# Performance work log

Hardware: AMD Instinct MI355X
Metric: run time of the kernel (lower is better)

## Reference

```python
import jax, jax.numpy as jnp
import numpy as np
from jax import lax

B, S, H, T = 64, 512, 1024, 48


def setup_inputs() -> dict:
    key = jax.random.key(0)
    ks = jax.random.split(key, 8)
    x = jax.random.normal(ks[0], (B, S, H), dtype=jnp.float32)
    # left-aligned variable-length attention mask (lengths in [S//2, S])
    lengths = jax.random.randint(ks[1], (B,), S // 2, S + 1)
    attention_mask = (jnp.arange(S)[None, :] < lengths[:, None]).astype(jnp.int32)
    labels = jax.random.randint(ks[2], (B, S), 0, T).astype(jnp.int64)
    # decoder Linear(H, T)
    W = jax.random.normal(ks[3], (H, T), dtype=jnp.float32) / np.sqrt(H)
    b = jnp.zeros((T,), dtype=jnp.float32)
    # CRF parameters (allennlp-style: transitions + start/end transitions)
    transitions = jax.random.normal(ks[4], (T, T), dtype=jnp.float32) * 0.1
    start_trans = jax.random.normal(ks[5], (T,), dtype=jnp.float32) * 0.1
    end_trans = jax.random.normal(ks[6], (T,), dtype=jnp.float32) * 0.1
    return {"x": x, "attention_mask": attention_mask, "labels": labels,
            "W": W, "b": b, "transitions": transitions,
            "start_trans": start_trans, "end_trans": end_trans}


def _log_partition(logits, mask, trans, start, end):
    # logits [B,S,T], mask [B,S] int. Returns logZ [B].
    alpha0 = start[None, :] + logits[:, 0]                     # [B,T]
    emits = jnp.moveaxis(logits[:, 1:], 1, 0)                  # [S-1,B,T]
    ms = mask[:, 1:].T                                         # [S-1,B]

    def step(alpha, inp):
        emit, m = inp
        inner = alpha[:, :, None] + trans[None, :, :] + emit[:, None, :]  # [B,T,T]
        new = jax.nn.logsumexp(inner, axis=1)
        alpha = jnp.where(m[:, None] > 0, new, alpha)
        return alpha, None

    alpha, _ = lax.scan(step, alpha0, (emits, ms))
    return jax.nn.logsumexp(alpha + end[None, :], axis=1)      # [B]


def _gold_score(logits, labels, mask, trans, start, end):
    maskf = mask.astype(logits.dtype)
    emit = jnp.take_along_axis(logits, labels[..., None], axis=2)[..., 0]  # [B,S]
    emit_score = jnp.sum(emit * maskf, axis=1)
    tr = trans[labels[:, :-1], labels[:, 1:]]                   # [B,S-1]
    trans_score = jnp.sum(tr * maskf[:, 1:], axis=1)
    last_idx = jnp.sum(mask, axis=1) - 1                        # [B]
    last_tags = jnp.take_along_axis(labels, last_idx[:, None], axis=1)[:, 0]
    return start[labels[:, 0]] + emit_score + trans_score + end[last_tags]


def _viterbi(logits, mask, trans, start, end):
    Bn, Sn, Tn = logits.shape
    v0 = start[None, :] + logits[:, 0]
    emits = jnp.moveaxis(logits[:, 1:], 1, 0)                  # [S-1,B,T]
    ms = mask[:, 1:].T
    ident = jnp.broadcast_to(jnp.arange(Tn, dtype=jnp.int32)[None, :], (Bn, Tn))

    def step(v, inp):
        emit, m = inp
        scores = v[:, :, None] + trans[None, :, :]              # [B,T_prev,T_cur]
        bp = jnp.argmax(scores, axis=1).astype(jnp.int32)       # [B,T]
        best = jnp.max(scores, axis=1) + emit
        v_new = jnp.where(m[:, None] > 0, best, v)
        bp = jnp.where(m[:, None] > 0, bp, ident)               # identity at padded steps
        return v_new, bp

    v, bps = lax.scan(step, v0, (emits, ms))                    # bps [S-1,B,T]
    last = jnp.argmax(v + end[None, :], axis=1).astype(jnp.int32)  # [B]

    def back(tag, bp):
        prev = jnp.take_along_axis(bp, tag[:, None], axis=1)[:, 0]
        return prev, tag

    first_tag, rest = lax.scan(back, last, bps, reverse=True)   # rest [S-1,B]
    tags = jnp.concatenate([first_tag[:, None], rest.T], axis=1)  # [B,S]
    return (tags * mask).astype(jnp.int64)                      # pad with zeros


def reference(x, attention_mask, labels, W, b, transitions, start_trans, end_trans):
    features = jnp.einsum('bsh,ht->bst', x, W) + b              # decoder Linear
    pred_labels = _viterbi(features, attention_mask, transitions, start_trans, end_trans)
    logZ = _log_partition(features, attention_mask, transitions, start_trans, end_trans)
    gold = _gold_score(features, labels, attention_mask, transitions, start_trans, end_trans)
    loss = -jnp.sum(gold - logZ)                                # -log-likelihood, summed over batch
    return features, pred_labels, loss
```

## Files before the change

kernel.cpp:

```cpp
#include <hip/hip_runtime.h>
#include <hip/hip_bf16.h>
#include <math.h>

#define Bn 64
#define Sn 512
#define Hn 1024
#define Tn 48

#define LOG2E 1.4426950408889634f
#define LN2f  0.6931471805599453f

#define PRED_OFF (Bn*Sn*Tn)
#define LOSS_OFF (PRED_OFF + Bn*Sn)

#define RL(x,i) __int_as_float(__builtin_amdgcn_readlane(__float_as_int(x),(i)))

#if __has_builtin(__builtin_amdgcn_exp2f)
#define EXP2(x) __builtin_amdgcn_exp2f(x)
#else
#define EXP2(x) exp2f(x)
#endif
#if __has_builtin(__builtin_amdgcn_logf)
#define LOG2(x) __builtin_amdgcn_logf(x)
#else
#define LOG2(x) log2f(x)
#endif

__device__ __forceinline__ unsigned umin2(unsigned a, unsigned b) { return a < b ? a : b; }

#define VWS_BYTE_OFF 512
#define BPW_BYTE_OFF (512 + (size_t)Bn*Sn*Tn*4)

#define DOT4(ACC,A,B) { ACC = fmaf((A).x,(B).x,ACC); ACC = fmaf((A).y,(B).y,ACC); ACC = fmaf((A).z,(B).z,ACC); ACC = fmaf((A).w,(B).w,ACC); }

__global__ __launch_bounds__(256) void gemm_feat(
    const float* __restrict__ x, const float* __restrict__ W,
    const float* __restrict__ bias, float* __restrict__ feat)
{
  __shared__ __align__(16) float xs[128][68];
  __shared__ __align__(16) float wsT[Tn][68];
  const int tid = threadIdx.x;
  const int srow  = tid >> 1;
  const int shalf = tid & 1;
  const int ty = tid >> 3;
  const int tx = tid & 7;
  const size_t row0 = (size_t)blockIdx.x * 128;

  float4 xreg[8];
  float  wreg[12];
  #pragma unroll
  for (int p = 0; p < 8; ++p)
    xreg[p] = *reinterpret_cast<const float4*>(&x[(row0 + srow)*Hn + shalf*32 + p*4]);
  #pragma unroll
  for (int i = 0; i < 12; ++i) {
    const int id = tid + i*256; const int kk = id/Tn; const int t = id - kk*Tn;
    wreg[i] = W[(size_t)kk*Tn + t];
  }

  float acc[4][6];
  #pragma unroll
  for (int r = 0; r < 4; ++r)
    #pragma unroll
    for (int c = 0; c < 6; ++c) acc[r][c] = 0.f;

  for (int k0 = 0; k0 < Hn; k0 += 64) {
    #pragma unroll
    for (int p = 0; p < 8; ++p)
      *reinterpret_cast<float4*>(&xs[srow][shalf*32 + p*4]) = xreg[p];
    #pragma unroll
    for (int i = 0; i < 12; ++i) {
      const int id = tid + i*256; const int kk = id/Tn; const int t = id - kk*Tn;
      wsT[t][kk] = wreg[i];
    }
    __syncthreads();
    if (k0 + 64 < Hn) {
      #pragma unroll
      for (int p = 0; p < 8; ++p)
        xreg[p] = *reinterpret_cast<const float4*>(&x[(row0 + srow)*Hn + (k0+64) + shalf*32 + p*4]);
      #pragma unroll
      for (int i = 0; i < 12; ++i) {
        const int id = tid + i*256; const int kk = id/Tn; const int t = id - kk*Tn;
        wreg[i] = W[(size_t)(k0 + 64 + kk)*Tn + t];
      }
    }
    #pragma unroll 4
    for (int kk = 0; kk < 64; kk += 4) {
      const float4 a0 = *reinterpret_cast<const float4*>(&xs[ty +  0][kk]);
      const float4 a1 = *reinterpret_cast<const float4*>(&xs[ty + 32][kk]);
      const float4 a2 = *reinterpret_cast<const float4*>(&xs[ty + 64][kk]);
      const float4 a3 = *reinterpret_cast<const float4*>(&xs[ty + 96][kk]);
      const float4 w0 = *reinterpret_cast<const float4*>(&wsT[tx*6+0][kk]);
      const float4 w1 = *reinterpret_cast<const float4*>(&wsT[tx*6+1][kk]);
      const float4 w2 = *reinterpret_cast<const float4*>(&wsT[tx*6+2][kk]);
      const float4 w3 = *reinterpret_cast<const float4*>(&wsT[tx*6+3][kk]);
      const float4 w4 = *reinterpret_cast<const float4*>(&wsT[tx*6+4][kk]);
      const float4 w5 = *reinterpret_cast<const float4*>(&wsT[tx*6+5][kk]);
      DOT4(acc[0][0],a0,w0) DOT4(acc[0][1],a0,w1) DOT4(acc[0][2],a0,w2)
      DOT4(acc[0][3],a0,w3) DOT4(acc[0][4],a0,w4) DOT4(acc[0][5],a0,w5)
      DOT4(acc[1][0],a1,w0) DOT4(acc[1][1],a1,w1) DOT4(acc[1][2],a1,w2)
      DOT4(acc[1][3],a1,w3) DOT4(acc[1][4],a1,w4) DOT4(acc[1][5],a1,w5)
      DOT4(acc[2][0],a2,w0) DOT4(acc[2][1],a2,w1) DOT4(acc[2][2],a2,w2)
      DOT4(acc[2][3],a2,w3) DOT4(acc[2][4],a2,w4) DOT4(acc[2][5],a2,w5)
      DOT4(acc[3][0],a3,w0) DOT4(acc[3][1],a3,w1) DOT4(acc[3][2],a3,w2)
      DOT4(acc[3][3],a3,w3) DOT4(acc[3][4],a3,w4) DOT4(acc[3][5],a3,w5)
    }
    __syncthreads();
  }
  #pragma unroll
  for (int c = 0; c < 6; ++c) {
    const int col = tx*6 + c;
    const float bv = bias[col];
    #pragma unroll
    for (int r = 0; r < 4; ++r)
      feat[(row0 + ty + r*32)*Tn + col] = acc[r][c] + bv;
  }
}

__device__ __forceinline__ int seq_len(const int* __restrict__ mask, int b, int lane) {
  int lc = 0;
  #pragma unroll
  for (int it = 0; it < Sn/64; ++it) lc += (mask[(size_t)b*Sn + it*64 + lane] != 0);
  #pragma unroll
  for (int off = 32; off; off >>= 1) lc += __shfl_xor(lc, off);
  return lc;
}

__global__ __launch_bounds__(64, 1) void crf_scan(
    const float* __restrict__ feat,
    const int* __restrict__ mask,
    const int* __restrict__ labels,
    const float* __restrict__ trans,
    const float* __restrict__ startv,
    const float* __restrict__ endv,
    float* __restrict__ vws,
    float* __restrict__ wsLogZ,
    float* __restrict__ wsGold)
{
  const int role = blockIdx.x >> 6;
  const int b    = blockIdx.x & 63;
  const int lane = threadIdx.x;
  const float* fb = feat + (size_t)b * Sn * Tn;
  const int len = seq_len(mask, b, lane);
  const int j = (lane < Tn) ? lane : (Tn - 1);

  if (role == 0) {
    float4 E0,E1,E2,E3,E4,E5,E6,E7,E8,E9,E10,E11;
    #define LDE(k) E##k.x = EXP2(trans[(4*k+0)*Tn + j]*LOG2E); \
                   E##k.y = EXP2(trans[(4*k+1)*Tn + j]*LOG2E); \
                   E##k.z = EXP2(trans[(4*k+2)*Tn + j]*LOG2E); \
                   E##k.w = EXP2(trans[(4*k+3)*Tn + j]*LOG2E);
    LDE(0) LDE(1) LDE(2) LDE(3) LDE(4) LDE(5) LDE(6) LDE(7) LDE(8) LDE(9) LDE(10) LDE(11)
    #undef LDE
    float emq0,emq1,emq2,emq3,emq4,emq5,emq6,emq7;
    #define LDEM(u) { int s = 1 + u; s = s < len ? s : len - 1; emq##u = fb[(size_t)s*Tn + j]; }
    LDEM(0) LDEM(1) LDEM(2) LDEM(3) LDEM(4) LDEM(5) LDEM(6) LDEM(7)
    #undef LDEM
    const float a0 = (startv[j] + fb[j]) * LOG2E;
    float Zref = RL(a0, 0);
    float beta = a0 - Zref;
    float p = EXP2(beta);
    #define FMAG(k) \
      s0 = fmaf(RL(p,4*k+0), E##k.x, s0); \
      s1 = fmaf(RL(p,4*k+1), E##k.y, s1); \
      s2 = fmaf(RL(p,4*k+2), E##k.z, s2); \
      s3 = fmaf(RL(p,4*k+3), E##k.w, s3);
    #define PSTEP(u) { const int tt = t + u; if (tt < len) { \
      const float em2 = emq##u * LOG2E; \
      int tf = tt + 8; tf = tf < len ? tf : len - 1; \
      emq##u = fb[(size_t)tf * Tn + j]; \
      float s0=0.f,s1=0.f,s2=0.f,s3=0.f; \
      FMAG(0) FMAG(1) FMAG(2) FMAG(3) FMAG(4) FMAG(5) \
      FMAG(6) FMAG(7) FMAG(8) FMAG(9) FMAG(10) FMAG(11) \
      const float dj = LOG2((s0+s1)+(s2+s3)) + em2; \
      const float d0 = RL(dj,0); \
      Zref += d0; beta = dj - d0; p = EXP2(beta); } }
    for (int t = 1; t < len; t += 8) {
      PSTEP(0) PSTEP(1) PSTEP(2) PSTEP(3) PSTEP(4) PSTEP(5) PSTEP(6) PSTEP(7)
    }
    #undef PSTEP
    #undef FMAG
    float fv = (lane < Tn) ? beta + endv[lane] * LOG2E : -INFINITY;
    float m = fv;
    #pragma unroll
    for (int off = 32; off; off >>= 1) m = fmaxf(m, __shfl_xor(m, off));
    float e = (lane < Tn) ? EXP2(fv - m) : 0.f;
    #pragma unroll
    for (int off = 32; off; off >>= 1) e += __shfl_xor(e, off);
    if (lane == 0) wsLogZ[b] = (Zref + m + LOG2(e)) * LN2f;

  } else if (role == 1) {
    float4 T0,T1,T2,T3,T4,T5,T6,T7,T8,T9,T10,T11;
    #define LDT(k) T##k.x = trans[(4*k+0)*Tn + j]; \
                   T##k.y = trans[(4*k+1)*Tn + j]; \
                   T##k.z = trans[(4*k+2)*Tn + j]; \
                   T##k.w = trans[(4*k+3)*Tn + j];
    LDT(0) LDT(1) LDT(2) LDT(3) LDT(4) LDT(5) LDT(6) LDT(7) LDT(8) LDT(9) LDT(10) LDT(11)
    #undef LDT
    float emq0,emq1,emq2,emq3,emq4,emq5,emq6,emq7;
    #define LDEM(u) { int s = 1 + u; s = s < len ? s : len - 1; emq##u = fb[(size_t)s*Tn + j]; }
    LDEM(0) LDEM(1) LDEM(2) LDEM(3) LDEM(4) LDEM(5) LDEM(6) LDEM(7)
    #undef LDEM
    float v = startv[j] + fb[j];
    if (lane < Tn) vws[(size_t)b*Sn*Tn + lane] = v;
    #define MAXG(k) const float g##k = fmaxf( \
      fmaxf(RL(v,4*k+0)+T##k.x, RL(v,4*k+1)+T##k.y), \
      fmaxf(RL(v,4*k+2)+T##k.z, RL(v,4*k+3)+T##k.w));
    #define VSTEP(u) { const int tt = t + u; if (tt < len) { \
      const float em_cur = emq##u; \
      int tf = tt + 8; tf = tf < len ? tf : len - 1; \
      emq##u = fb[(size_t)tf * Tn + j]; \
      MAXG(0) MAXG(1) MAXG(2) MAXG(3) MAXG(4) MAXG(5) \
      MAXG(6) MAXG(7) MAXG(8) MAXG(9) MAXG(10) MAXG(11) \
      const float h0 = fmaxf(fmaxf(g0,g1),fmaxf(g2,g3)); \
      const float h1 = fmaxf(fmaxf(g4,g5),fmaxf(g6,g7)); \
      const float h2 = fmaxf(fmaxf(g8,g9),fmaxf(g10,g11)); \
      const float best = fmaxf(fmaxf(h0,h1),h2); \
      v = best + em_cur; \
      if (lane < Tn) vws[((size_t)b*Sn + tt)*Tn + lane] = v; } }
    for (int t = 1; t < len; t += 8) {
      VSTEP(0) VSTEP(1) VSTEP(2) VSTEP(3) VSTEP(4) VSTEP(5) VSTEP(6) VSTEP(7)
    }
    #undef VSTEP
    #undef MAXG

  } else {
    float g = 0.f;
    #pragma unroll
    for (int it = 0; it < Sn/64; ++it) {
      const int sg = it*64 + lane;
      if (sg < len) {
        const int la = labels[(size_t)b*Sn + sg];
        float e = fb[(size_t)sg*Tn + la];
        if (sg > 0) e += trans[labels[(size_t)b*Sn + sg - 1]*Tn + la];
        g += e;
      }
    }
    #pragma unroll
    for (int off = 32; off; off >>= 1) g += __shfl_xor(g, off);
    if (lane == 0) {
      g += startv[labels[(size_t)b*Sn]] + endv[labels[(size_t)b*Sn + len - 1]];
      wsGold[b] = g;
    }
  }
}

__global__ __launch_bounds__(256) void bp_kernel(
    const float* __restrict__ vws,
    const int* __restrict__ mask,
    const float* __restrict__ trans,
    unsigned char* __restrict__ bpw)
{
  const int b    = blockIdx.x >> 3;
  const int oct  = blockIdx.x & 7;
  const int wv   = threadIdx.x >> 6;
  const int lane = threadIdx.x & 63;
  const int len = seq_len(mask, b, lane);
  const int j = (lane < Tn) ? lane : (Tn - 1);

  float4 T0,T1,T2,T3,T4,T5,T6,T7,T8,T9,T10,T11;
  #define LDT(k) T##k.x = trans[(4*k+0)*Tn + j]; \
                 T##k.y = trans[(4*k+1)*Tn + j]; \
                 T##k.z = trans[(4*k+2)*Tn + j]; \
                 T##k.w = trans[(4*k+3)*Tn + j];
  LDT(0) LDT(1) LDT(2) LDT(3) LDT(4) LDT(5) LDT(6) LDT(7) LDT(8) LDT(9) LDT(10) LDT(11)
  #undef LDT

  const int t0 = oct*64 + wv*16;
  for (int i = 0; i < 16; ++i) {
    const int t = t0 + i;
    int te = t; te = te < 1 ? 1 : te; te = te < len ? te : len - 1;
    const float4* vp = reinterpret_cast<const float4*>(vws + ((size_t)b*Sn + te - 1)*Tn);
    #define LDA(k) const float4 A##k = vp[k];
    LDA(0) LDA(1) LDA(2) LDA(3) LDA(4) LDA(5) LDA(6) LDA(7) LDA(8) LDA(9) LDA(10) LDA(11)
    #undef LDA
    #define GMAX(k) const float gq##k = fmaxf( \
      fmaxf(A##k.x+T##k.x, A##k.y+T##k.y), fmaxf(A##k.z+T##k.z, A##k.w+T##k.w));
    GMAX(0) GMAX(1) GMAX(2) GMAX(3) GMAX(4) GMAX(5)
    GMAX(6) GMAX(7) GMAX(8) GMAX(9) GMAX(10) GMAX(11)
    #undef GMAX
    const float h0 = fmaxf(fmaxf(gq0,gq1),fmaxf(gq2,gq3));
    const float h1 = fmaxf(fmaxf(gq4,gq5),fmaxf(gq6,gq7));
    const float h2 = fmaxf(fmaxf(gq8,gq9),fmaxf(gq10,gq11));
    const float best = fmaxf(fmaxf(h0,h1),h2);
    #define KEYG(k) umin2( \
      umin2(__float_as_uint((A##k.x+T##k.x)-best)|(unsigned)(4*k+0), \
            __float_as_uint((A##k.y+T##k.y)-best)|(unsigned)(4*k+1)), \
      umin2(__float_as_uint((A##k.z+T##k.z)-best)|(unsigned)(4*k+2), \
            __float_as_uint((A##k.w+T##k.w)-best)|(unsigned)(4*k+3)))
    const unsigned kA = umin2(umin2(KEYG(0), KEYG(1)), umin2(KEYG(2), KEYG(3)));
    const unsigned kB = umin2(umin2(KEYG(4), KEYG(5)), umin2(KEYG(6), KEYG(7)));
    const unsigned kC = umin2(umin2(KEYG(8), KEYG(9)), umin2(KEYG(10), KEYG(11)));
    #undef KEYG
    const unsigned bidx = umin2(umin2(kA, kB), kC);
    if (t >= 1 && t < len && lane < Tn)
      bpw[((size_t)b*Sn + t)*Tn + lane] = (unsigned char)bidx;
  }
}

__device__ __forceinline__ unsigned idw(int a) {
  return (unsigned)a | ((unsigned)(a+1)<<8) | ((unsigned)(a+2)<<16) | ((unsigned)(a+3)<<24);
}

__global__ __launch_bounds__(64, 1) void backtrace_kernel(
    const float* __restrict__ vws,
    const unsigned char* __restrict__ bpw,
    const int* __restrict__ mask,
    const float* __restrict__ endv,
    float* __restrict__ pred_out)
{
  __shared__ unsigned char bpL[Sn * Tn];
  __shared__ unsigned char pathL[384 * 64];
  __shared__ int EA[8];

  const int b    = blockIdx.x;
  const int lane = threadIdx.x;
  const int len = seq_len(mask, b, lane);

  {
    const uint4* gb = reinterpret_cast<const uint4*>(bpw + (size_t)b*Sn*Tn);
    uint4* bl = reinterpret_cast<uint4*>(bpL);
    for (int i4 = lane; i4 < Sn*Tn/16; i4 += 64) {
      const int byte0 = i4*16;
      const int t = byte0 / Tn;
      const int j0 = byte0 - t*Tn;
      uint4 val;
      if (t >= 1 && t < len) val = gb[i4];
      else { val.x = idw(j0); val.y = idw(j0+4); val.z = idw(j0+8); val.w = idw(j0+12); }
      bl[i4] = val;
    }
  }

  float fv = (lane < Tn) ? vws[((size_t)b*Sn + len - 1)*Tn + lane] + endv[lane] : -INFINITY;
  int fi = (lane < Tn) ? lane : 64;
  #pragma unroll
  for (int off = 32; off; off >>= 1) {
    const float ov = __shfl_xor(fv, off);
    const int   oi = __shfl_xor(fi, off);
    if (ov > fv || (ov == fv && oi < fi)) { fv = ov; fi = oi; }
  }
  __syncthreads();

  #define JOB(r) \
    const int id##r  = lane + 64*(r); \
    const int seg##r = id##r & 7;     \
    int cur##r = id##r >> 3;          \
    const int bpb##r = seg##r * 64 * Tn; \
    const int pb##r  = id##r << 6;    \
    pathL[pb##r + 63] = (unsigned char)cur##r;
  JOB(0) JOB(1) JOB(2) JOB(3) JOB(4) JOB(5)
  for (int d = 62; d >= 0; --d) {
    const int o = (d + 1) * Tn;
    cur0 = bpL[bpb0 + o + cur0]; pathL[pb0 + d] = (unsigned char)cur0;
    cur1 = bpL[bpb1 + o + cur1]; pathL[pb1 + d] = (unsigned char)cur1;
    cur2 = bpL[bpb2 + o + cur2]; pathL[pb2 + d] = (unsigned char)cur2;
    cur3 = bpL[bpb3 + o + cur3]; pathL[pb3 + d] = (unsigned char)cur3;
    cur4 = bpL[bpb4 + o + cur4]; pathL[pb4 + d] = (unsigned char)cur4;
    cur5 = bpL[bpb5 + o + cur5]; pathL[pb5 + d] = (unsigned char)cur5;
  }
  #undef JOB
  __syncthreads();
  if (lane == 0) {
    int Ecur = fi;
    EA[7] = Ecur;
    for (int s = 7; s >= 1; --s) {
      const int bottom = pathL[((Ecur << 3) + s) * 64];
      Ecur = bpL[(s * 64) * Tn + bottom];
      EA[s-1] = Ecur;
    }
  }
  __syncthreads();
  #pragma unroll
  for (int r8 = 0; r8 < 8; ++r8) {
    const int t = r8*64 + lane;
    const int pv = pathL[((EA[r8] << 3) + r8) * 64 + lane];
    pred_out[(size_t)b*Sn + t] = (t < len) ? (float)pv : 0.f;
  }
}

__global__ void loss_reduce(const float* __restrict__ wsLogZ,
                            const float* __restrict__ wsGold,
                            float* __restrict__ out)
{
  const int lane = threadIdx.x;
  float v = wsLogZ[lane] - wsGold[lane];
  #pragma unroll
  for (int off = 32; off; off >>= 1) v += __shfl_xor(v, off);
  if (lane == 0) out[0] = v;
}

extern "C" void kernel_launch(void* const* d_in, const int* in_sizes, int n_in,
                              void* d_out, int out_size, void* d_ws, size_t ws_size,
                              hipStream_t stream) {
  const float* x      = (const float*)d_in[0];
  const int*   mask   = (const int*)  d_in[1];
  const int*   labels = (const int*)  d_in[2];
  const float* W      = (const float*)d_in[3];
  const float* bias   = (const float*)d_in[4];
  const float* trans  = (const float*)d_in[5];
  const float* startv = (const float*)d_in[6];
  const float* endv   = (const float*)d_in[7];

  float* out  = (float*)d_out;
  float* feat = out;
  float* pred = out + PRED_OFF;
  float* loss = out + LOSS_OFF;
  float* wsLogZ = (float*)d_ws;
  float* wsGold = wsLogZ + 64;
  float* vws = (float*)((char*)d_ws + VWS_BYTE_OFF);
  unsigned char* bpw = (unsigned char*)d_ws + BPW_BYTE_OFF;

  gemm_feat<<<(Bn*Sn)/128, 256, 0, stream>>>(x, W, bias, feat);
  crf_scan<<<192, 64, 0, stream>>>(feat, mask, labels, trans, startv, endv, vws, wsLogZ, wsGold);
  bp_kernel<<<512, 256, 0, stream>>>(vws, mask, trans, bpw);
  backtrace_kernel<<<64, 64, 0, stream>>>(vws, bpw, mask, endv, pred);
  loss_reduce<<<1, 64, 0, stream>>>(wsLogZ, wsGold, loss);
}
```

Baseline: 398.6 us.

## Shrink GEMM row tile and move CRF state broadcast to LDS

The feature GEMM now uses 64-row tiles instead of 128, doubling the grid to 512 blocks to improve CU occupancy for a memory-bound matmul. The CRF forward and Viterbi scans stop broadcasting the per-tag state with 48 readlane ops per step. Instead they write the state to LDS each step and read it back as float4 vectors alongside a transposed, padded transition (or exp-transition) table kept in LDS. This trades SALU/readlane serialization for LDS traffic. It relies on in-wave ordering of LDS writes and reads within a single 64-lane wave and adds no barrier per step.

```diff
diff --git a/kernel.cpp b/kernel.cpp
--- a/kernel.cpp
+++ b/kernel.cpp
@@ -37,36 +37,36 @@
     const float* __restrict__ x, const float* __restrict__ W,
     const float* __restrict__ bias, float* __restrict__ feat)
 {
-  __shared__ __align__(16) float xs[128][68];
+  __shared__ __align__(16) float xs[64][68];
   __shared__ __align__(16) float wsT[Tn][68];
   const int tid = threadIdx.x;
-  const int srow  = tid >> 1;
-  const int shalf = tid & 1;
+  const int srow = tid >> 2;
+  const int sqc  = tid & 3;
   const int ty = tid >> 3;
   const int tx = tid & 7;
-  const size_t row0 = (size_t)blockIdx.x * 128;
-
-  float4 xreg[8];
+  const size_t row0 = (size_t)blockIdx.x * 64;
+
+  float4 xreg[4];
   float  wreg[12];
   #pragma unroll
-  for (int p = 0; p < 8; ++p)
-    xreg[p] = *reinterpret_cast<const float4*>(&x[(row0 + srow)*Hn + shalf*32 + p*4]);
+  for (int p = 0; p < 4; ++p)
+    xreg[p] = *reinterpret_cast<const float4*>(&x[(row0 + srow)*Hn + (sqc + p*4)*4]);
   #pragma unroll
   for (int i = 0; i < 12; ++i) {
     const int id = tid + i*256; const int kk = id/Tn; const int t = id - kk*Tn;
     wreg[i] = W[(size_t)kk*Tn + t];
   }
 
-  float acc[4][6];
-  #pragma unroll
-  for (int r = 0; r < 4; ++r)
+  float acc[2][6];
+  #pragma unroll
+  for (int r = 0; r < 2; ++r)
     #pragma unroll
     for (int c = 0; c < 6; ++c) acc[r][c] = 0.f;
 
   for (int k0 = 0; k0 < Hn; k0 += 64) {
     #pragma unroll
-    for (int p = 0; p < 8; ++p)
-      *reinterpret_cast<float4*>(&xs[srow][shalf*32 + p*4]) = xreg[p];
+    for (int p = 0; p < 4; ++p)
+      *reinterpret_cast<float4*>(&xs[srow][(sqc + p*4)*4]) = xreg[p];
     #pragma unroll
     for (int i = 0; i < 12; ++i) {
       const int id = tid + i*256; const int kk = id/Tn; const int t = id - kk*Tn;
@@ -75,8 +75,8 @@
     __syncthreads();
     if (k0 + 64 < Hn) {
       #pragma unroll
-      for (int p = 0; p < 8; ++p)
-        xreg[p] = *reinterpret_cast<const float4*>(&x[(row0 + srow)*Hn + (k0+64) + shalf*32 + p*4]);
+      for (int p = 0; p < 4; ++p)
+        xreg[p] = *reinterpret_cast<const float4*>(&x[(row0 + srow)*Hn + (k0+64) + (sqc + p*4)*4]);
       #pragma unroll
       for (int i = 0; i < 12; ++i) {
         const int id = tid + i*256; const int kk = id/Tn; const int t = id - kk*Tn;
@@ -85,10 +85,8 @@
     }
     #pragma unroll 4
     for (int kk = 0; kk < 64; kk += 4) {
-      const float4 a0 = *reinterpret_cast<const float4*>(&xs[ty +  0][kk]);
-      const float4 a1 = *reinterpret_cast<const float4*>(&xs[ty + 32][kk]);
-      const float4 a2 = *reinterpret_cast<const float4*>(&xs[ty + 64][kk]);
-      const float4 a3 = *reinterpret_cast<const float4*>(&xs[ty + 96][kk]);
+      const float4 a0 = *reinterpret_cast<const float4*>(&xs[ty*2+0][kk]);
+      const float4 a1 = *reinterpret_cast<const float4*>(&xs[ty*2+1][kk]);
       const float4 w0 = *reinterpret_cast<const float4*>(&wsT[tx*6+0][kk]);
       const float4 w1 = *reinterpret_cast<const float4*>(&wsT[tx*6+1][kk]);
       const float4 w2 = *reinterpret_cast<const float4*>(&wsT[tx*6+2][kk]);
@@ -99,10 +97,6 @@
       DOT4(acc[0][3],a0,w3) DOT4(acc[0][4],a0,w4) DOT4(acc[0][5],a0,w5)
       DOT4(acc[1][0],a1,w0) DOT4(acc[1][1],a1,w1) DOT4(acc[1][2],a1,w2)
       DOT4(acc[1][3],a1,w3) DOT4(acc[1][4],a1,w4) DOT4(acc[1][5],a1,w5)
-      DOT4(acc[2][0],a2,w0) DOT4(acc[2][1],a2,w1) DOT4(acc[2][2],a2,w2)
-      DOT4(acc[2][3],a2,w3) DOT4(acc[2][4],a2,w4) DOT4(acc[2][5],a2,w5)
-      DOT4(acc[3][0],a3,w0) DOT4(acc[3][1],a3,w1) DOT4(acc[3][2],a3,w2)
-      DOT4(acc[3][3],a3,w3) DOT4(acc[3][4],a3,w4) DOT4(acc[3][5],a3,w5)
     }
     __syncthreads();
   }
@@ -111,8 +105,8 @@
     const int col = tx*6 + c;
     const float bv = bias[col];
     #pragma unroll
-    for (int r = 0; r < 4; ++r)
-      feat[(row0 + ty + r*32)*Tn + col] = acc[r][c] + bv;
+    for (int r = 0; r < 2; ++r)
+      feat[(row0 + ty*2 + r)*Tn + col] = acc[r][c] + bv;
   }
 }
 
@@ -124,6 +118,8 @@
   for (int off = 32; off; off >>= 1) lc += __shfl_xor(lc, off);
   return lc;
 }
+
+#define ETS 52
 
 __global__ __launch_bounds__(64, 1) void crf_scan(
     const float* __restrict__ feat,
@@ -136,6 +132,8 @@
     float* __restrict__ wsLogZ,
     float* __restrict__ wsGold)
 {
+  __shared__ __align__(16) float LB[64 + 48*ETS];
+
   const int role = blockIdx.x >> 6;
   const int b    = blockIdx.x & 63;
   const int lane = threadIdx.x;
@@ -143,14 +141,15 @@
   const int len = seq_len(mask, b, lane);
   const int j = (lane < Tn) ? lane : (Tn - 1);
 
+  const float4* sv4 = reinterpret_cast<const float4*>(&LB[0]);
+  const float4* et4 = reinterpret_cast<const float4*>(&LB[64 + j*ETS]);
+
   if (role == 0) {
-    float4 E0,E1,E2,E3,E4,E5,E6,E7,E8,E9,E10,E11;
-    #define LDE(k) E##k.x = EXP2(trans[(4*k+0)*Tn + j]*LOG2E); \
-                   E##k.y = EXP2(trans[(4*k+1)*Tn + j]*LOG2E); \
-                   E##k.z = EXP2(trans[(4*k+2)*Tn + j]*LOG2E); \
-                   E##k.w = EXP2(trans[(4*k+3)*Tn + j]*LOG2E);
-    LDE(0) LDE(1) LDE(2) LDE(3) LDE(4) LDE(5) LDE(6) LDE(7) LDE(8) LDE(9) LDE(10) LDE(11)
-    #undef LDE
+    for (int idx = lane; idx < Tn*Tn; idx += 64) {
+      const int ii = idx / Tn, jj = idx - (idx/Tn)*Tn;
+      LB[64 + jj*ETS + ii] = EXP2(trans[idx] * LOG2E);
+    }
+    __syncthreads();
     float emq0,emq1,emq2,emq3,emq4,emq5,emq6,emq7;
     #define LDEM(u) { int s = 1 + u; s = s < len ? s : len - 1; emq##u = fb[(size_t)s*Tn + j]; }
     LDEM(0) LDEM(1) LDEM(2) LDEM(3) LDEM(4) LDEM(5) LDEM(6) LDEM(7)
@@ -158,27 +157,29 @@
     const float a0 = (startv[j] + fb[j]) * LOG2E;
     float Zref = RL(a0, 0);
     float beta = a0 - Zref;
-    float p = EXP2(beta);
-    #define FMAG(k) \
-      s0 = fmaf(RL(p,4*k+0), E##k.x, s0); \
-      s1 = fmaf(RL(p,4*k+1), E##k.y, s1); \
-      s2 = fmaf(RL(p,4*k+2), E##k.z, s2); \
-      s3 = fmaf(RL(p,4*k+3), E##k.w, s3);
+    LB[lane] = EXP2(beta);
     #define PSTEP(u) { const int tt = t + u; if (tt < len) { \
       const float em2 = emq##u * LOG2E; \
       int tf = tt + 8; tf = tf < len ? tf : len - 1; \
       emq##u = fb[(size_t)tf * Tn + j]; \
       float s0=0.f,s1=0.f,s2=0.f,s3=0.f; \
-      FMAG(0) FMAG(1) FMAG(2) FMAG(3) FMAG(4) FMAG(5) \
-      FMAG(6) FMAG(7) FMAG(8) FMAG(9) FMAG(10) FMAG(11) \
+      _Pragma("unroll") \
+      for (int r = 0; r < 12; ++r) { \
+        const float4 pv = sv4[r]; \
+        const float4 ev = et4[r]; \
+        s0 = fmaf(pv.x, ev.x, s0); \
+        s1 = fmaf(pv.y, ev.y, s1); \
+        s2 = fmaf(pv.z, ev.z, s2); \
+        s3 = fmaf(pv.w, ev.w, s3); \
+      } \
       const float dj = LOG2((s0+s1)+(s2+s3)) + em2; \
       const float d0 = RL(dj,0); \
-      Zref += d0; beta = dj - d0; p = EXP2(beta); } }
+      Zref += d0; beta = dj - d0; \
+      LB[lane] = EXP2(beta); } }
     for (int t = 1; t < len; t += 8) {
       PSTEP(0) PSTEP(1) PSTEP(2) PSTEP(3) PSTEP(4) PSTEP(5) PSTEP(6) PSTEP(7)
     }
     #undef PSTEP
-    #undef FMAG
     float fv = (lane < Tn) ? beta + endv[lane] * LOG2E : -INFINITY;
     float m = fv;
     #pragma unroll
@@ -189,39 +190,40 @@
     if (lane == 0) wsLogZ[b] = (Zref + m + LOG2(e)) * LN2f;
 
   } else if (role == 1) {
-    float4 T0,T1,T2,T3,T4,T5,T6,T7,T8,T9,T10,T11;
-    #define LDT(k) T##k.x = trans[(4*k+0)*Tn + j]; \
-                   T##k.y = trans[(4*k+1)*Tn + j]; \
-                   T##k.z = trans[(4*k+2)*Tn + j]; \
-                   T##k.w = trans[(4*k+3)*Tn + j];
-    LDT(0) LDT(1) LDT(2) LDT(3) LDT(4) LDT(5) LDT(6) LDT(7) LDT(8) LDT(9) LDT(10) LDT(11)
-    #undef LDT
+    for (int idx = lane; idx < Tn*Tn; idx += 64) {
+      const int ii = idx / Tn, jj = idx - (idx/Tn)*Tn;
+      LB[64 + jj*ETS + ii] = trans[idx];
+    }
+    __syncthreads();
     float emq0,emq1,emq2,emq3,emq4,emq5,emq6,emq7;
     #define LDEM(u) { int s = 1 + u; s = s < len ? s : len - 1; emq##u = fb[(size_t)s*Tn + j]; }
     LDEM(0) LDEM(1) LDEM(2) LDEM(3) LDEM(4) LDEM(5) LDEM(6) LDEM(7)
     #undef LDEM
     float v = startv[j] + fb[j];
+    LB[lane] = v;
     if (lane < Tn) vws[(size_t)b*Sn*Tn + lane] = v;
-    #define MAXG(k) const float g##k = fmaxf( \
-      fmaxf(RL(v,4*k+0)+T##k.x, RL(v,4*k+1)+T##k.y), \
-      fmaxf(RL(v,4*k+2)+T##k.z, RL(v,4*k+3)+T##k.w));
     #define VSTEP(u) { const int tt = t + u; if (tt < len) { \
       const float em_cur = emq##u; \
       int tf = tt + 8; tf = tf < len ? tf : len - 1; \
       emq##u = fb[(size_t)tf * Tn + j]; \
-      MAXG(0) MAXG(1) MAXG(2) MAXG(3) MAXG(4) MAXG(5) \
-      MAXG(6) MAXG(7) MAXG(8) MAXG(9) MAXG(10) MAXG(11) \
-      const float h0 = fmaxf(fmaxf(g0,g1),fmaxf(g2,g3)); \
-      const float h1 = fmaxf(fmaxf(g4,g5),fmaxf(g6,g7)); \
-      const float h2 = fmaxf(fmaxf(g8,g9),fmaxf(g10,g11)); \
-      const float best = fmaxf(fmaxf(h0,h1),h2); \
+      float g0 = -INFINITY, g1 = -INFINITY, g2 = -INFINITY, g3 = -INFINITY; \
+      _Pragma("unroll") \
+      for (int r = 0; r < 12; ++r) { \
+        const float4 pv = sv4[r]; \
+        const float4 tv = et4[r]; \
+        g0 = fmaxf(g0, pv.x + tv.x); \
+        g1 = fmaxf(g1, pv.y + tv.y); \
+        g2 = fmaxf(g2, pv.z + tv.z); \
+        g3 = fmaxf(g3, pv.w + tv.w); \
+      } \
+      const float best = fmaxf(fmaxf(g0,g1), fmaxf(g2,g3)); \
       v = best + em_cur; \
+      LB[lane] = v; \
       if (lane < Tn) vws[((size_t)b*Sn + tt)*Tn + lane] = v; } }
     for (int t = 1; t < len; t += 8) {
       VSTEP(0) VSTEP(1) VSTEP(2) VSTEP(3) VSTEP(4) VSTEP(5) VSTEP(6) VSTEP(7)
     }
     #undef VSTEP
-    #undef MAXG
 
   } else {
     float g = 0.f;
@@ -409,7 +411,7 @@
   float* vws = (float*)((char*)d_ws + VWS_BYTE_OFF);
   unsigned char* bpw = (unsigned char*)d_ws + BPW_BYTE_OFF;
 
-  gemm_feat<<<(Bn*Sn)/128, 256, 0, stream>>>(x, W, bias, feat);
+  gemm_feat<<<(Bn*Sn)/64, 256, 0, stream>>>(x, W, bias, feat);
   crf_scan<<<192, 64, 0, stream>>>(feat, mask, labels, trans, startv, endv, vws, wsLogZ, wsGold);
   bp_kernel<<<512, 256, 0, stream>>>(vws, mask, trans, bpw);
   backtrace_kernel<<<64, 64, 0, stream>>>(vws, bpw, mask, endv, pred);
```

Result: faster. 343.1 us (-13.9%).
